# Kernel optimization log

Measured on AMD Instinct MI355X. Metric: run time of the kernel, lower is better.

## Reference

```python
import jax, jax.numpy as jnp
import numpy as np

N_NODES = 50000
N_EDGES = 800000
IN_CH = 128
HID = 32
HEADS = 4
OUT_CH = 10
N_GRAPHS = 64
NEG_SLOPE = 0.2  # PyG GATConv default


def setup_inputs() -> dict:
    key = jax.random.key(0)
    ks = jax.random.split(key, 16)
    d = {}
    d["x"] = jax.random.normal(ks[0], (N_NODES, IN_CH), dtype=jnp.float32)
    d["edge_index"] = jax.random.randint(ks[1], (2, N_EDGES), 0, N_NODES, dtype=jnp.int64)
    d["batch"] = jnp.sort(jax.random.randint(ks[2], (N_NODES,), 0, N_GRAPHS, dtype=jnp.int64))
    s1 = 1.0 / np.sqrt(IN_CH)
    s2 = 1.0 / np.sqrt(HEADS * HID)
    d["W1"] = jax.random.normal(ks[3], (IN_CH, HEADS * HID), dtype=jnp.float32) * s1
    d["att_src1"] = jax.random.normal(ks[4], (HEADS, HID), dtype=jnp.float32) * s2
    d["att_dst1"] = jax.random.normal(ks[5], (HEADS, HID), dtype=jnp.float32) * s2
    d["b1"] = jnp.zeros((HEADS * HID,), dtype=jnp.float32)
    d["W2"] = jax.random.normal(ks[6], (HEADS * HID, HEADS * HID), dtype=jnp.float32) * s2
    d["att_src2"] = jax.random.normal(ks[7], (HEADS, HID), dtype=jnp.float32) * s2
    d["att_dst2"] = jax.random.normal(ks[8], (HEADS, HID), dtype=jnp.float32) * s2
    d["b2"] = jnp.zeros((HEADS * HID,), dtype=jnp.float32)
    d["w_lin"] = jax.random.normal(ks[9], (HEADS * HID, OUT_CH), dtype=jnp.float32) * s2
    d["b_lin"] = jnp.zeros((OUT_CH,), dtype=jnp.float32)
    return d


def _gat_conv(x, src, dst, W, att_src, att_dst, bias):
    # x: [N, Fin] -> h: [N, H, C]
    h = (x @ W).reshape(N_NODES, HEADS, HID)
    a_src = jnp.sum(h * att_src, axis=-1)  # [N, H]
    a_dst = jnp.sum(h * att_dst, axis=-1)  # [N, H]
    e = jax.nn.leaky_relu(a_src[src] + a_dst[dst], NEG_SLOPE)  # [E, H]
    # segment softmax over incoming edges of each destination node
    e_max = jax.ops.segment_max(e, dst, num_segments=N_NODES)  # [N, H]
    e_exp = jnp.exp(e - e_max[dst])
    denom = jax.ops.segment_sum(e_exp, dst, num_segments=N_NODES)  # [N, H]
    alpha = e_exp / denom[dst]  # [E, H]
    # weighted scatter-add aggregation
    out = jax.ops.segment_sum(alpha[:, :, None] * h[src], dst, num_segments=N_NODES)
    return out.reshape(N_NODES, HEADS * HID) + bias


def reference(x, edge_index, batch, W1, att_src1, att_dst1, b1,
              W2, att_src2, att_dst2, b2, w_lin, b_lin):
    # PyG GATConv adds self loops by default
    loops = jnp.arange(N_NODES, dtype=edge_index.dtype)
    src = jnp.concatenate([edge_index[0], loops])
    dst = jnp.concatenate([edge_index[1], loops])

    h = jax.nn.relu(_gat_conv(x, src, dst, W1, att_src1, att_dst1, b1))
    h = jax.nn.relu(_gat_conv(h, src, dst, W2, att_src2, att_dst2, b2))

    # global mean pool over graphs
    sums = jax.ops.segment_sum(h, batch, num_segments=N_GRAPHS)  # [G, H*C]
    counts = jax.ops.segment_sum(jnp.ones((N_NODES,), dtype=h.dtype), batch,
                                 num_segments=N_GRAPHS)
    pooled = sums / jnp.maximum(counts, 1.0)[:, None]

    # dropout is identity in eval mode
    return pooled @ w_lin + b_lin
```

## Files before the change

kernel.cpp:

```cpp
#include <hip/hip_runtime.h>
#include <hip/hip_bf16.h>
#include <math.h>

constexpr int NN = 50000;
constexpr int NE = 800000;
constexpr int ET = NE + NN;
constexpr int FH = 128;
constexpr int NHEAD = 4;
constexpr int NG = 64;
constexpr int OC = 10;

constexpr int NBK = (NN + 255) >> 8;
constexpr int EPB = 4000;
constexpr int HBLK = NE / EPB;

constexpr int WKP = 136;
constexpr int WPLANE = 128 * WKP;

constexpr int GEMM1_GRID = (NN + 255) / 256;
constexpr int GEMM2_GRID = (NN + 255) / 256;

typedef __attribute__((ext_vector_type(8))) short short8;
typedef __attribute__((ext_vector_type(4))) float f32x4;

__device__ inline ushort f2bf_bits(float f) {
    union { __hip_bfloat16 h; ushort u; } c;
    c.h = __float2bfloat16(f);
    return c.u;
}

#define GEMM_EPILOGUE()                                                          \
    float as_[8], ad_[8];                                                        \
    _Pragma("unroll")                                                            \
    for (int t = 0; t < 8; ++t) {                                                \
        as_[t] = att_s[t * 16 + l16];                                            \
        ad_[t] = att_d[t * 16 + l16];                                            \
    }                                                                            \
    float hs[4][4], hd[4][4];                                                    \
    _Pragma("unroll")                                                            \
    for (int r = 0; r < 4; ++r) {                                                \
        int grow = row0 + quad * 4 + r;                                          \
        bool okr = (grow < NN);                                                  \
        _Pragma("unroll")                                                        \
        for (int h = 0; h < 4; ++h) {                                            \
            hs[r][h] = acc[2*h][r] * as_[2*h] + acc[2*h+1][r] * as_[2*h+1];      \
            hd[r][h] = acc[2*h][r] * ad_[2*h] + acc[2*h+1][r] * ad_[2*h+1];      \
        }                                                                        \
        if (okr) {                                                               \
            _Pragma("unroll")                                                    \
            for (int t = 0; t < 8; ++t)                                          \
                Hb[(size_t)grow * FH + t * 16 + l16] = __float2bfloat16(acc[t][r]); \
        }                                                                        \
    }                                                                            \
    _Pragma("unroll")                                                            \
    for (int o = 1; o < 16; o <<= 1) {                                           \
        _Pragma("unroll")                                                        \
        for (int r = 0; r < 4; ++r)                                              \
            _Pragma("unroll")                                                    \
            for (int h = 0; h < 4; ++h) {                                        \
                hs[r][h] += __shfl_xor(hs[r][h], o);                             \
                hd[r][h] += __shfl_xor(hd[r][h], o);                             \
            }                                                                    \
    }                                                                            \
    if (l16 == 0) {                                                              \
        _Pragma("unroll")                                                        \
        for (int r = 0; r < 4; ++r) {                                            \
            int grow = row0 + quad * 4 + r;                                      \
            if (grow < NN) {                                                     \
                *(float4*)&a_src[grow * NHEAD] = make_float4(hs[r][0], hs[r][1], hs[r][2], hs[r][3]); \
                *(float4*)&a_dst[grow * NHEAD] = make_float4(hd[r][0], hd[r][1], hd[r][2], hd[r][3]); \
            }                                                                    \
        }                                                                        \
    }

__global__ __launch_bounds__(1024) void fused_gemm_hist_kernel(
    const int* __restrict__ ei, int* __restrict__ blockHist,
    const float* __restrict__ A, const float* __restrict__ W1,
    const float* __restrict__ W2, ushort* __restrict__ wt,
    const float* __restrict__ att_s, const float* __restrict__ att_d,
    __hip_bfloat16* __restrict__ Hb, float* __restrict__ a_src, float* __restrict__ a_dst)
{
    __shared__ __align__(16) ushort Wlds[2 * WPLANE];
    const int tid = threadIdx.x;

    if (blockIdx.x >= GEMM1_GRID) {
        const int blk = blockIdx.x - GEMM1_GRID;
        int* hist = (int*)Wlds;
        if (tid < NBK) hist[tid] = 0;
        __syncthreads();
        const int e0 = blk * EPB;
        if (tid < EPB / 4) {
            int4 d4 = *(const int4*)(ei + NE + e0 + 4 * tid);
            atomicAdd(&hist[d4.x >> 8], 1);
            atomicAdd(&hist[d4.y >> 8], 1);
            atomicAdd(&hist[d4.z >> 8], 1);
            atomicAdd(&hist[d4.w >> 8], 1);
        }
        if (blk < 64 && tid < 256) {
            int idx = blk * 256 + tid;
            int k = idx >> 7, n = idx & 127;
            float f = W2[idx];
            ushort hb = f2bf_bits(f);
            union { ushort u; __hip_bfloat16 h; } c; c.u = hb;
            float lo = f - __bfloat162float(c.h);
            wt[n * WKP + k] = hb;
            wt[WPLANE + n * WKP + k] = f2bf_bits(lo);
        }
        __syncthreads();
        if (tid < NBK) blockHist[tid * HBLK + blk] = hist[tid];
        return;
    }

    for (int i = tid; i < FH * 128; i += 1024) {
        int k = i >> 7, n = i & 127;
        float f = W1[i];
        ushort hb = f2bf_bits(f);
        union { ushort u; __hip_bfloat16 h; } c; c.u = hb;
        float lo = f - __bfloat162float(c.h);
        Wlds[n * WKP + k] = hb;
        Wlds[WPLANE + n * WKP + k] = f2bf_bits(lo);
    }
    __syncthreads();

    const int wave = tid >> 6;
    const int lane = tid & 63;
    const int quad = lane >> 4;
    const int l16 = lane & 15;
    const int row0 = blockIdx.x * 256 + wave * 16;

    f32x4 acc[8];
#pragma unroll
    for (int t = 0; t < 8; ++t) acc[t] = (f32x4){0.f, 0.f, 0.f, 0.f};

    int arow = row0 + l16; if (arow >= NN) arow = NN - 1;
    const float* ap = A + (size_t)arow * FH + quad * 8;

#pragma unroll
    for (int kc = 0; kc < 4; ++kc) {
        float4 x0 = *(const float4*)(ap + kc * 32);
        float4 x1 = *(const float4*)(ap + kc * 32 + 4);
        float av[8] = {x0.x, x0.y, x0.z, x0.w, x1.x, x1.y, x1.z, x1.w};
        short8 ah, al;
#pragma unroll
        for (int j = 0; j < 8; ++j) {
            ushort hb = f2bf_bits(av[j]);
            union { ushort u; __hip_bfloat16 h; } c; c.u = hb;
            float lo = av[j] - __bfloat162float(c.h);
            ah[j] = (short)hb;
            al[j] = (short)f2bf_bits(lo);
        }
        const int kof = kc * 32 + quad * 8;
#pragma unroll
        for (int t = 0; t < 8; ++t) {
            const ushort* wp = &Wlds[(t * 16 + l16) * WKP + kof];
            short8 wh = *(const short8*)wp;
            short8 wl = *(const short8*)(wp + WPLANE);
            acc[t] = __builtin_amdgcn_mfma_f32_16x16x32_bf16(ah, wh, acc[t], 0, 0, 0);
            acc[t] = __builtin_amdgcn_mfma_f32_16x16x32_bf16(al, wh, acc[t], 0, 0, 0);
            acc[t] = __builtin_amdgcn_mfma_f32_16x16x32_bf16(ah, wl, acc[t], 0, 0, 0);
        }
    }
    GEMM_EPILOGUE()
}

__global__ __launch_bounds__(1024) void bucket_scatter_kernel(
    const int* __restrict__ ei, const int* __restrict__ bh,
    int* __restrict__ ebase, int* __restrict__ offs,
    int2* __restrict__ ebuf) {
    __shared__ int sd[256];
    __shared__ int cur[NBK];
    const int tid = threadIdx.x;
    const int blk = blockIdx.x;

    int total = 0, pre = 0;
    if (tid < NBK) {
        const int* p = bh + tid * HBLK;
        for (int j = 0; j < HBLK; ++j) {
            int v = p[j];
            pre += (j < blk) ? v : 0;
            total += v;
        }
    }
    if (tid < 256) sd[tid] = (tid < NBK) ? total : 0;
    __syncthreads();
    for (int o = 1; o < 256; o <<= 1) {
        int u = (tid < 256 && tid >= o) ? sd[tid - o] : 0;
        __syncthreads();
        if (tid < 256) sd[tid] += u;
        __syncthreads();
    }
    if (tid < NBK) {
        const int base = sd[tid] - total;
        cur[tid] = base + pre;
        if (blk == 0) {
            ebase[tid] = base;
            if (tid == NBK - 1) { ebase[NBK] = sd[tid]; offs[NN] = ET; }
        }
    }
    __syncthreads();

    const int e0 = blk * EPB;
    if (tid < EPB / 4) {
        int4 d4 = *(const int4*)(ei + NE + e0 + 4 * tid);
        int4 s4 = *(const int4*)(ei + e0 + 4 * tid);
        int ds[4] = {d4.x, d4.y, d4.z, d4.w};
        int ss[4] = {s4.x, s4.y, s4.z, s4.w};
#pragma unroll
        for (int j = 0; j < 4; ++j) {
            int pos = atomicAdd(&cur[ds[j] >> 8], 1);
            ebuf[pos] = make_int2(ss[j], ds[j]);
        }
    }
}

__global__ __launch_bounds__(256) void bucket_csr_kernel(
    const int2* __restrict__ ebuf, const int* __restrict__ ebase,
    int* __restrict__ offs, int* __restrict__ csrc) {
    __shared__ int hist[256];
    __shared__ int sd[256];
    __shared__ int cur[256];
    const int b = blockIdx.x, t = threadIdx.x;
    const int lo = b << 8;
    int psz = NN - lo; if (psz > 256) psz = 256;
    const int e0 = ebase[b], e1 = ebase[b + 1];

    hist[t] = 0;
    __syncthreads();
    for (int k = e0 + t; k < e1; k += 256) {
        int2 e = ebuf[k];
        atomicAdd(&hist[e.y - lo], 1);
    }
    __syncthreads();
    const int d = hist[t];
    sd[t] = d; __syncthreads();
#pragma unroll
    for (int o = 1; o < 256; o <<= 1) {
        int u = (t >= o) ? sd[t - o] : 0;
        __syncthreads();
        sd[t] += u;
        __syncthreads();
    }
    const int ex = sd[t] - d;
    if (t < psz) {
        const int node = lo + t;
        const int o = e0 + ex + node;
        offs[node] = o;
        cur[t] = o;
        csrc[o + d] = node;
    }
    __syncthreads();
    for (int k = e0 + t; k < e1; k += 256) {
        int2 e = ebuf[k];
        int pos = atomicAdd(&cur[e.y - lo], 1);
        csrc[pos] = e.x;
    }
}

__global__ __launch_bounds__(1024) void gemm_att_bf16_kernel(
    const __hip_bfloat16* __restrict__ A, const ushort* __restrict__ wt,
    const float* __restrict__ att_s, const float* __restrict__ att_d,
    __hip_bfloat16* __restrict__ Hb, float* __restrict__ a_src, float* __restrict__ a_dst)
{
    __shared__ __align__(16) ushort Wlds[2 * WPLANE];
    const int tid = threadIdx.x;
    {
        const uint4* s = (const uint4*)wt;
        uint4* d = (uint4*)Wlds;
        for (int i = tid; i < 2 * WPLANE / 8; i += 1024) d[i] = s[i];
    }
    __syncthreads();

    const int wave = tid >> 6;
    const int lane = tid & 63;
    const int quad = lane >> 4;
    const int l16 = lane & 15;
    const int row0 = blockIdx.x * 256 + wave * 16;

    f32x4 acc[8];
#pragma unroll
    for (int t = 0; t < 8; ++t) acc[t] = (f32x4){0.f, 0.f, 0.f, 0.f};

    int arow = row0 + l16; if (arow >= NN) arow = NN - 1;
    const __hip_bfloat16* ap = A + (size_t)arow * FH + quad * 8;

#pragma unroll
    for (int kc = 0; kc < 4; ++kc) {
        short8 ah = *(const short8*)(ap + kc * 32);
        const int kof = kc * 32 + quad * 8;
#pragma unroll
        for (int t = 0; t < 8; ++t) {
            const ushort* wp = &Wlds[(t * 16 + l16) * WKP + kof];
            short8 wh = *(const short8*)wp;
            short8 wl = *(const short8*)(wp + WPLANE);
            acc[t] = __builtin_amdgcn_mfma_f32_16x16x32_bf16(ah, wh, acc[t], 0, 0, 0);
            acc[t] = __builtin_amdgcn_mfma_f32_16x16x32_bf16(ah, wl, acc[t], 0, 0, 0);
        }
    }
    GEMM_EPILOGUE()
}

__global__ __launch_bounds__(256) void gat_agg_kernel(
    const __hip_bfloat16* __restrict__ Hb, const float* __restrict__ asrc,
    const float* __restrict__ adst, const int* __restrict__ offs,
    const int* __restrict__ csrc, const float* __restrict__ bias,
    __hip_bfloat16* __restrict__ out)
{
    const int wid = threadIdx.x >> 6;
    const int lane = threadIdx.x & 63;
    const int n = blockIdx.x * 4 + wid;

    const int beg = offs[n], end = offs[n + 1];
    const int es = lane >> 4;
    const int fs = lane & 15;
    const int hC = fs >> 2;
    const int f8 = fs * 8;
    const float adC = adst[n * NHEAD + hC];

    float dsum = 0.f;
    float acc[8];
#pragma unroll
    for (int i = 0; i < 8; ++i) acc[i] = 0.f;

    const int last = end - 1;
    const int n8 = (end - beg + 7) >> 3;
    for (int p = 0; p < n8; ++p) {
        const int eA = beg + 8 * p + es;
        const int eB = eA + 4;
        const bool vA = eA < end, vB = eB < end;
        const int sA = csrc[vA ? eA : last];
        const int sB = csrc[vB ? eB : last];
        float aA = asrc[sA * NHEAD + hC] + adC;
        float aB = asrc[sB * NHEAD + hC] + adC;
        aA = aA > 0.f ? aA : 0.2f * aA;
        aB = aB > 0.f ? aB : 0.2f * aB;
        const float wA = vA ? __expf(aA) : 0.f;
        const float wB = vB ? __expf(aB) : 0.f;
        dsum += wA + wB;
        union { uint4 u; __hip_bfloat162 b[4]; } cvA, cvB;
        cvA.u = *(const uint4*)&Hb[(size_t)sA * FH + f8];
        cvB.u = *(const uint4*)&Hb[(size_t)sB * FH + f8];
#pragma unroll
        for (int i = 0; i < 4; ++i) {
            float2 hA = __bfloat1622float2(cvA.b[i]);
            float2 hB2 = __bfloat1622float2(cvB.b[i]);
            acc[2 * i]     = fmaf(wA, hA.x, acc[2 * i]);
            acc[2 * i + 1] = fmaf(wA, hA.y, acc[2 * i + 1]);
            acc[2 * i]     = fmaf(wB, hB2.x, acc[2 * i]);
            acc[2 * i + 1] = fmaf(wB, hB2.y, acc[2 * i + 1]);
        }
    }
    dsum += __shfl_xor(dsum, 1);
    dsum += __shfl_xor(dsum, 2);
    dsum += __shfl_xor(dsum, 16);
    dsum += __shfl_xor(dsum, 32);
#pragma unroll
    for (int i = 0; i < 8; ++i) {
        acc[i] += __shfl_xor(acc[i], 16);
        acc[i] += __shfl_xor(acc[i], 32);
    }
    const float inv = 4.0f / dsum;
    if (es == 0) {
        union { ushort u8[8]; uint4 u; } pk;
#pragma unroll
        for (int i = 0; i < 8; ++i) {
            float v = fmaxf(fmaf(acc[i], inv, bias[f8 + i]), 0.f);
            pk.u8[i] = f2bf_bits(v);
        }
        *(uint4*)&out[(size_t)n * FH + f8] = pk.u;
    }
}

__global__ __launch_bounds__(256) void pool_final_kernel(
    const __hip_bfloat16* __restrict__ X, const int* __restrict__ batch,
    const float* __restrict__ wl, const float* __restrict__ bl,
    float* __restrict__ out)
{
    const int g = blockIdx.x;
    const int t = threadIdx.x;
    int a = 0, b = NN;
    while (a < b) { int m = (a + b) >> 1; if (batch[m] < g) a = m + 1; else b = m; }
    const int gs = a;
    b = NN;
    while (a < b) { int m = (a + b) >> 1; if (batch[m] <= g) a = m + 1; else b = m; }
    const int ge = a;

    const int rg = t >> 4;
    const int l16 = t & 15;
    float acc[8];
#pragma unroll
    for (int i = 0; i < 8; ++i) acc[i] = 0.f;
    for (int r = gs + rg; r < ge; r += 16) {
        union { uint4 u; __hip_bfloat162 bb[4]; } cv;
        cv.u = *(const uint4*)&X[(size_t)r * FH + l16 * 8];
#pragma unroll
        for (int i = 0; i < 4; ++i) {
            float2 f = __bfloat1622float2(cv.bb[i]);
            acc[2 * i]     += f.x;
            acc[2 * i + 1] += f.y;
        }
    }
    __shared__ float red[16][128];
    __shared__ float pl[128];
#pragma unroll
    for (int i = 0; i < 8; ++i) red[rg][l16 * 8 + i] = acc[i];
    __syncthreads();
    if (t < 128) {
        float s = 0.f;
#pragma unroll
        for (int j = 0; j < 16; ++j) s += red[j][t];
        pl[t] = s;
    }
    __syncthreads();
    if (t < OC) {
        float invc = 1.0f / fmaxf((float)(ge - gs), 1.0f);
        float a2 = 0.f;
        for (int k = 0; k < FH; ++k)
            a2 = fmaf(pl[k], wl[k * OC + t], a2);
        out[g * OC + t] = a2 * invc + bl[t];
    }
}

extern "C" void kernel_launch(void* const* d_in, const int* in_sizes, int n_in,
                              void* d_out, int out_size, void* d_ws, size_t ws_size,
                              hipStream_t stream) {
    const float* x       = (const float*)d_in[0];
    const int*   ei      = (const int*)d_in[1];
    const int*   batch   = (const int*)d_in[2];
    const float* W1      = (const float*)d_in[3];
    const float* as1     = (const float*)d_in[4];
    const float* ad1     = (const float*)d_in[5];
    const float* b1      = (const float*)d_in[6];
    const float* W2      = (const float*)d_in[7];
    const float* as2     = (const float*)d_in[8];
    const float* ad2     = (const float*)d_in[9];
    const float* b2      = (const float*)d_in[10];
    const float* wlin    = (const float*)d_in[11];
    const float* blin    = (const float*)d_in[12];
    float* out = (float*)d_out;

    __hip_bfloat16* hbuf = (__hip_bfloat16*)d_ws;
    __hip_bfloat16* abuf = hbuf + (size_t)NN * FH;
    float* asrc  = (float*)(abuf + (size_t)NN * FH);
    float* adst  = asrc + (size_t)NN * NHEAD;
    int* offs    = (int*)(adst + (size_t)NN * NHEAD);
    int* csrc    = offs + NN + 1;
    int2* ebuf   = (int2*)(((uintptr_t)(csrc + ET) + 7) & ~(uintptr_t)7);
    int* bh      = (int*)(ebuf + NE);
    int* ebase   = bh + NBK * HBLK;
    ushort* wt   = (ushort*)(((uintptr_t)(ebase + NBK + 1) + 15) & ~(uintptr_t)15);

    fused_gemm_hist_kernel<<<GEMM1_GRID + HBLK, 1024, 0, stream>>>(
        ei, bh, x, W1, W2, wt, as1, ad1, hbuf, asrc, adst);

    bucket_scatter_kernel<<<HBLK, 1024, 0, stream>>>(ei, bh, ebase, offs, ebuf);
    bucket_csr_kernel<<<NBK, 256, 0, stream>>>(ebuf, ebase, offs, csrc);

    const int agg_grid = NN / 4;

    gat_agg_kernel<<<agg_grid, 256, 0, stream>>>(hbuf, asrc, adst, offs, csrc, b1, abuf);
    gemm_att_bf16_kernel<<<GEMM2_GRID, 1024, 0, stream>>>(abuf, wt, as2, ad2, hbuf, asrc, adst);
    gat_agg_kernel<<<agg_grid, 256, 0, stream>>>(hbuf, asrc, adst, offs, csrc, b2, abuf);

    pool_final_kernel<<<NG, 256, 0, stream>>>(abuf, batch, wlin, blin, out);
}
```

Measured before the change: 246.3 us.

## Use nontemporal loads for streamed data and widen bucket CSR blocks

Replaces ordinary loads with nontemporal loads for streamed data: edge indices in the scatter, GEMM A rows, CSR source indices in aggregation, and features in pooling. The goal is to keep this single-use data from pushing reused data out of cache. Separately, the bucket CSR kernel now runs 1024 threads per block instead of 256, so the per-bucket edge loops need fewer iterations. The cost is idle threads and extra guards during the 256-wide prefix scan. Nontemporal hints could hurt where data is actually reused, for example the CSR indices, which are read again by the second aggregation pass.

```diff
diff --git a/kernel.cpp b/kernel.cpp
--- a/kernel.cpp
+++ b/kernel.cpp
@@ -22,11 +22,17 @@
 
 typedef __attribute__((ext_vector_type(8))) short short8;
 typedef __attribute__((ext_vector_type(4))) float f32x4;
+typedef __attribute__((ext_vector_type(4))) int int4x;
+typedef __attribute__((ext_vector_type(4))) unsigned int uint4x;
 
 __device__ inline ushort f2bf_bits(float f) {
     union { __hip_bfloat16 h; ushort u; } c;
     c.h = __float2bfloat16(f);
     return c.u;
+}
+
+__device__ inline int4x nt_load_i4(const int* p) {
+    return __builtin_nontemporal_load((const int4x*)p);
 }
 
 #define GEMM_EPILOGUE()                                                          \
@@ -201,19 +207,17 @@
 
     const int e0 = blk * EPB;
     if (tid < EPB / 4) {
-        int4 d4 = *(const int4*)(ei + NE + e0 + 4 * tid);
-        int4 s4 = *(const int4*)(ei + e0 + 4 * tid);
-        int ds[4] = {d4.x, d4.y, d4.z, d4.w};
-        int ss[4] = {s4.x, s4.y, s4.z, s4.w};
+        int4x d4 = nt_load_i4(ei + NE + e0 + 4 * tid);
+        int4x s4 = nt_load_i4(ei + e0 + 4 * tid);
 #pragma unroll
         for (int j = 0; j < 4; ++j) {
-            int pos = atomicAdd(&cur[ds[j] >> 8], 1);
-            ebuf[pos] = make_int2(ss[j], ds[j]);
-        }
-    }
-}
-
-__global__ __launch_bounds__(256) void bucket_csr_kernel(
+            int pos = atomicAdd(&cur[d4[j] >> 8], 1);
+            ebuf[pos] = make_int2(s4[j], d4[j]);
+        }
+    }
+}
+
+__global__ __launch_bounds__(1024) void bucket_csr_kernel(
     const int2* __restrict__ ebuf, const int* __restrict__ ebase,
     int* __restrict__ offs, int* __restrict__ csrc) {
     __shared__ int hist[256];
@@ -224,32 +228,32 @@
     int psz = NN - lo; if (psz > 256) psz = 256;
     const int e0 = ebase[b], e1 = ebase[b + 1];
 
-    hist[t] = 0;
-    __syncthreads();
-    for (int k = e0 + t; k < e1; k += 256) {
+    if (t < 256) hist[t] = 0;
+    __syncthreads();
+    for (int k = e0 + t; k < e1; k += 1024) {
         int2 e = ebuf[k];
         atomicAdd(&hist[e.y - lo], 1);
     }
     __syncthreads();
-    const int d = hist[t];
-    sd[t] = d; __syncthreads();
-#pragma unroll
+    const int d = (t < 256) ? hist[t] : 0;
+    if (t < 256) sd[t] = d;
+    __syncthreads();
     for (int o = 1; o < 256; o <<= 1) {
-        int u = (t >= o) ? sd[t - o] : 0;
-        __syncthreads();
-        sd[t] += u;
-        __syncthreads();
-    }
-    const int ex = sd[t] - d;
+        int u = (t < 256 && t >= o) ? sd[t - o] : 0;
+        __syncthreads();
+        if (t < 256) sd[t] += u;
+        __syncthreads();
+    }
     if (t < psz) {
+        const int ex = sd[t] - d;
         const int node = lo + t;
-        const int o = e0 + ex + node;
-        offs[node] = o;
-        cur[t] = o;
-        csrc[o + d] = node;
-    }
-    __syncthreads();
-    for (int k = e0 + t; k < e1; k += 256) {
+        const int o2 = e0 + ex + node;
+        offs[node] = o2;
+        cur[t] = o2;
+        csrc[o2 + d] = node;
+    }
+    __syncthreads();
+    for (int k = e0 + t; k < e1; k += 1024) {
         int2 e = ebuf[k];
         int pos = atomicAdd(&cur[e.y - lo], 1);
         csrc[pos] = e.x;
@@ -285,7 +289,7 @@
 
 #pragma unroll
     for (int kc = 0; kc < 4; ++kc) {
-        short8 ah = *(const short8*)(ap + kc * 32);
+        short8 ah = __builtin_nontemporal_load((const short8*)(ap + kc * 32));
         const int kof = kc * 32 + quad * 8;
 #pragma unroll
         for (int t = 0; t < 8; ++t) {
@@ -327,8 +331,8 @@
         const int eA = beg + 8 * p + es;
         const int eB = eA + 4;
         const bool vA = eA < end, vB = eB < end;
-        const int sA = csrc[vA ? eA : last];
-        const int sB = csrc[vB ? eB : last];
+        const int sA = __builtin_nontemporal_load(&csrc[vA ? eA : last]);
+        const int sB = __builtin_nontemporal_load(&csrc[vB ? eB : last]);
         float aA = asrc[sA * NHEAD + hC] + adC;
         float aB = asrc[sB * NHEAD + hC] + adC;
         aA = aA > 0.f ? aA : 0.2f * aA;
@@ -390,8 +394,8 @@
 #pragma unroll
     for (int i = 0; i < 8; ++i) acc[i] = 0.f;
     for (int r = gs + rg; r < ge; r += 16) {
-        union { uint4 u; __hip_bfloat162 bb[4]; } cv;
-        cv.u = *(const uint4*)&X[(size_t)r * FH + l16 * 8];
+        union { uint4x u; __hip_bfloat162 bb[4]; } cv;
+        cv.u = __builtin_nontemporal_load((const uint4x*)&X[(size_t)r * FH + l16 * 8]);
 #pragma unroll
         for (int i = 0; i < 4; ++i) {
             float2 f = __bfloat1622float2(cv.bb[i]);
@@ -453,7 +457,7 @@
         ei, bh, x, W1, W2, wt, as1, ad1, hbuf, asrc, adst);
 
     bucket_scatter_kernel<<<HBLK, 1024, 0, stream>>>(ei, bh, ebase, offs, ebuf);
-    bucket_csr_kernel<<<NBK, 256, 0, stream>>>(ebuf, ebase, offs, csrc);
+    bucket_csr_kernel<<<NBK, 1024, 0, stream>>>(ebuf, ebase, offs, csrc);
 
     const int agg_grid = NN / 4;
 
```

Measured after the change: 246.2 us. No clear change (-0.0%).
